# Performance work log

Hardware: AMD Instinct MI355X
Metric: run time of the kernel (lower is better)

## Reference

```python
import jax, jax.numpy as jnp
import numpy as np

B, H, S, D = 4, 16, 1024, 64
MAX_REL = 16  # max_relative_position


def setup_inputs() -> dict:
    key = jax.random.key(0)
    kq, kk, kv, kr = jax.random.split(key, 4)
    Q = jax.random.normal(kq, (B, H, S, D), dtype=jnp.float32)
    K = jax.random.normal(kk, (B, H, S, D), dtype=jnp.float32)
    V = jax.random.normal(kv, (B, H, S, D), dtype=jnp.float32)
    # learned relative-position embedding table [2*P+1, d_k]
    rel_table = jax.random.normal(kr, (2 * MAX_REL + 1, D), dtype=jnp.float32) * 0.02
    # causal mask, broadcastable over batch/heads; 0 => masked
    mask = jnp.tril(jnp.ones((S, S), dtype=jnp.int32))[None, None, :, :]
    return {"Q": Q, "K": K, "V": V, "rel_table": rel_table, "mask": mask}


def reference(Q, K, V, rel_table, mask):
    scale = jnp.sqrt(jnp.asarray(Q.shape[-1], Q.dtype))
    seq_len = Q.shape[2]
    r = jnp.arange(seq_len)
    # clipped relative distances -> embedding indices in [0, 2P]
    idx = jnp.clip(r[None, :] - r[:, None], -MAX_REL, MAX_REL) + MAX_REL  # [S,S]
    rel_emb = rel_table[idx]  # [S, S, D]
    scores = jnp.einsum('bhld,bhrd->bhlr', Q, K) / scale  # [B,H,S,S]
    scores = scores + jnp.einsum('bhld,lrd->bhlr', Q, rel_emb)
    scores = jnp.where(mask == 0, -jnp.inf, scores)
    attn = jax.nn.softmax(scores, axis=-1)
    output = jnp.einsum('bhlr,bhrd->bhld', attn, V)  # [B,H,S,D]
    return (output, attn)
```

## Files before the change

### kernel.cpp

```cpp
#include <hip/hip_runtime.h>

#define S_ 1024
#define D_ 64
#define RT 16
#define SCP 1036

typedef _Float16 f16x4 __attribute__((ext_vector_type(4)));
typedef _Float16 f16x8 __attribute__((ext_vector_type(8)));
typedef __fp16  h16x2 __attribute__((ext_vector_type(2)));
typedef float f32x4 __attribute__((ext_vector_type(4)));

__global__ __launch_bounds__(256)
void prep_kv(const float* __restrict__ K, const float* __restrict__ V,
             _Float16* __restrict__ Kws, _Float16* __restrict__ VT) {
    if (blockIdx.x < 1024) {
        const int idx = blockIdx.x * 256 + threadIdx.x;
        const int g4  = idx & 3;
        const float* kp = K + (size_t)(idx >> 2) * 64 + g4 * 16;
        _Float16* dst = Kws + (size_t)(idx >> 2) * 64 + g4 * 16;
        f16x8 o0, o1;
        #pragma unroll
        for (int u = 0; u < 2; ++u) {
            float4 f0 = *reinterpret_cast<const float4*>(kp + 8 * u);
            float4 f1 = *reinterpret_cast<const float4*>(kp + 8 * u + 4);
            f16x8& o = u ? o1 : o0;
            o[0] = (_Float16)f0.x; o[1] = (_Float16)f0.y;
            o[2] = (_Float16)f0.z; o[3] = (_Float16)f0.w;
            o[4] = (_Float16)f1.x; o[5] = (_Float16)f1.y;
            o[6] = (_Float16)f1.z; o[7] = (_Float16)f1.w;
        }
        *reinterpret_cast<f16x8*>(dst)     = o0;
        *reinterpret_cast<f16x8*>(dst + 8) = o1;
    } else {
        const int idx = (blockIdx.x - 1024) * 256 + threadIdx.x;
        const int bh  = idx >> 12;
        const int kt  = (idx >> 6) & 63;
        const int col = idx & 63;
        const float* vp = V + ((size_t)bh * S_ + kt * 16) * D_ + col;
        _Float16* dst = VT + ((size_t)(bh * 64 + kt) * 64 + col) * 16;
        f16x8 a, b;
        #pragma unroll
        for (int kk = 0; kk < 16; ++kk) {
            float f = vp[(size_t)kk * D_];
            if (kk < 8) a[kk] = (_Float16)f; else b[kk - 8] = (_Float16)f;
        }
        *reinterpret_cast<f16x8*>(dst)     = a;
        *reinterpret_cast<f16x8*>(dst + 8) = b;
    }
}

__global__ __launch_bounds__(256, 4)
void relattn_main(const float* __restrict__ Q, const float* __restrict__ rel,
                  const _Float16* __restrict__ Kws, const _Float16* __restrict__ VT,
                  float* __restrict__ outO, float* outA) {
    __shared__ __align__(16) _Float16 sc[RT * SCP];
    __shared__ float qrel[RT * 17];
    __shared__ float rowsum[4][RT];

    const int tid  = threadIdx.x;
    const int lane = tid & 63;
    const int w    = tid >> 6;
    const int l15  = lane & 15;
    const int g4   = lane >> 4;
    const int bid  = blockIdx.x;
    const int bh   = (bid & 7) + 8 * (bid >> 9);
    const int tile = 63 - ((bid >> 3) & 63);
    const int R0   = tile * RT;
    const int nt16 = tile + 1;
    const int bound = 16 * nt16;

    const float* Qb = Q + (size_t)bh * S_ * D_;
    const _Float16* Kb = Kws + (size_t)bh * 64 * 1024;
    const _Float16* Vt = VT  + (size_t)bh * 64 * 1024;

    {
        const int mend = (bound + 255) & ~255;
        const f16x8 zz = {0, 0, 0, 0, 0, 0, 0, 0};
        const int r = tid >> 4;
        for (int c = bound + (tid & 15) * 8; c < mend; c += 128)
            *reinterpret_cast<f16x8*>(&sc[r * SCP + c]) = zz;
    }

    {
        int idx = tid;
        #pragma unroll
        for (int rep = 0; rep < 2; ++rep) {
            if (idx < RT * 17) {
                const int i = idx / 17;
                const int j = idx - i * 17;
                const float* qp = Qb + (size_t)(R0 + i) * D_;
                const float* rp = rel + j * D_;
                float s = 0.f;
                #pragma unroll
                for (int d = 0; d < D_; d += 4) {
                    float4 a = *reinterpret_cast<const float4*>(qp + d);
                    float4 b = *reinterpret_cast<const float4*>(rp + d);
                    s += a.x * b.x + a.y * b.y + a.z * b.z + a.w * b.w;
                }
                qrel[idx] = s;
            }
            idx = 256 + tid;
        }
    }

    f16x8 aq0, aq1;
    {
        const float* qp = Qb + (size_t)(R0 + l15) * D_ + 8 * g4;
        float4 f0 = *reinterpret_cast<const float4*>(qp);
        float4 f1 = *reinterpret_cast<const float4*>(qp + 4);
        float4 f2 = *reinterpret_cast<const float4*>(qp + 32);
        float4 f3 = *reinterpret_cast<const float4*>(qp + 36);
        aq0 = f16x8{(_Float16)(f0.x*0.125f), (_Float16)(f0.y*0.125f),
                    (_Float16)(f0.z*0.125f), (_Float16)(f0.w*0.125f),
                    (_Float16)(f1.x*0.125f), (_Float16)(f1.y*0.125f),
                    (_Float16)(f1.z*0.125f), (_Float16)(f1.w*0.125f)};
        aq1 = f16x8{(_Float16)(f2.x*0.125f), (_Float16)(f2.y*0.125f),
                    (_Float16)(f2.z*0.125f), (_Float16)(f2.w*0.125f),
                    (_Float16)(f3.x*0.125f), (_Float16)(f3.y*0.125f),
                    (_Float16)(f3.z*0.125f), (_Float16)(f3.w*0.125f)};
    }

    const int myrow   = R0 + l15;
    const int fastmax = (R0 - 31) >> 4;

    auto k_load = [&](int ct, f16x8* kf) {
        const _Float16* kp = Kb + ((size_t)ct * 16 + l15) * 64 + 8 * g4;
        kf[0] = *reinterpret_cast<const f16x8*>(kp);
        kf[1] = *reinterpret_cast<const f16x8*>(kp + 32);
    };
    auto v_load = [&](int ct, f16x4* vf) {
        const _Float16* vp = Vt + ((size_t)ct * 64 + l15) * 16 + 4 * g4;
        #pragma unroll
        for (int n = 0; n < 4; ++n)
            vf[n] = *reinterpret_cast<const f16x4*>(vp + (size_t)n * 256);
    };
    auto load2 = [&](int ct0, f16x8* kf, f16x4* vf) {
        k_load(ct0, kf);
        v_load(ct0, vf);
        if (ct0 + 4 < nt16) { k_load(ct0 + 4, kf + 2); v_load(ct0 + 4, vf + 4); }
    };

    f16x8 kA[4], kB[4];
    f16x4 vA[8], vB[8];
    load2(w, kA, vA);

    __syncthreads();

    const float qr0 = qrel[l15 * 17];
    float psum = 0.f;
    f32x4 oa[4] = {{0,0,0,0},{0,0,0,0},{0,0,0,0},{0,0,0,0}};

    auto comp_tile = [&](int ct, const f16x8* kf, const f16x4* vf) {
        f32x4 acc = {0.f, 0.f, 0.f, 0.f};
        acc = __builtin_amdgcn_mfma_f32_16x16x32_f16(kf[0], aq0, acc, 0, 0, 0);
        acc = __builtin_amdgcn_mfma_f32_16x16x32_f16(kf[1], aq1, acc, 0, 0, 0);
        float e[4];
        if (ct <= fastmax) {
            #pragma unroll
            for (int j = 0; j < 4; ++j) e[j] = __expf(acc[j] + qr0);
        } else {
            #pragma unroll
            for (int j = 0; j < 4; ++j) {
                const int dlt = myrow - (ct * 16 + 4 * g4 + j);
                e[j] = 0.f;
                if (dlt >= 0)
                    e[j] = __expf(acc[j] + ((dlt < 16) ? qrel[l15 * 17 + 16 - dlt]
                                                       : qr0));
            }
        }
        psum += (e[0] + e[1]) + (e[2] + e[3]);
        h16x2 lo = __builtin_amdgcn_cvt_pkrtz(e[0], e[1]);
        h16x2 hi = __builtin_amdgcn_cvt_pkrtz(e[2], e[3]);
        f16x4 pk = {(_Float16)lo[0], (_Float16)lo[1],
                    (_Float16)hi[0], (_Float16)hi[1]};
        *reinterpret_cast<f16x4*>(&sc[l15 * SCP + ct * 16 + 4 * g4]) = pk;
        #pragma unroll
        for (int n = 0; n < 4; ++n)
            oa[n] = __builtin_amdgcn_mfma_f32_16x16x16f16(pk, vf[n], oa[n], 0, 0, 0);
    };
    auto comp2 = [&](int ct0, const f16x8* kf, const f16x4* vf) {
        comp_tile(ct0, kf, vf);
        if (ct0 + 4 < nt16) comp_tile(ct0 + 4, kf + 2, vf + 4);
    };

    for (int c0 = w; c0 < nt16; c0 += 16) {
        if (c0 + 8 < nt16) load2(c0 + 8, kB, vB);
        comp2(c0, kA, vA);
        if (c0 + 8 < nt16) {
            if (c0 + 16 < nt16) load2(c0 + 16, kA, vA);
            comp2(c0 + 8, kB, vB);
        }
    }

    psum += __shfl_xor(psum, 16);
    psum += __shfl_xor(psum, 32);
    if (lane < 16) rowsum[w][lane] = psum;
    __syncthreads();

    float* Ab = outA + ((size_t)bh * S_ + R0) * S_;
    #pragma unroll
    for (int ii = 0; ii < 4; ++ii) {
        const int i = 4 * w + ii;
        const float iv = 1.f / (rowsum[0][i] + rowsum[1][i] +
                                rowsum[2][i] + rowsum[3][i]);
        #pragma unroll
        for (int q = 0; q < 4; ++q) {
            const int c = q * 256 + lane * 4;
            f32x4 o = {0.f, 0.f, 0.f, 0.f};
            if (q * 256 < bound) {
                f16x4 sv = *reinterpret_cast<f16x4*>(&sc[i * SCP + c]);
                o = {(float)sv[0] * iv, (float)sv[1] * iv,
                     (float)sv[2] * iv, (float)sv[3] * iv};
            }
            __builtin_nontemporal_store(
                o, reinterpret_cast<f32x4*>(Ab + (size_t)i * S_ + c));
        }
    }

    __syncthreads();

    float* Opart = reinterpret_cast<float*>(sc);
    #pragma unroll
    for (int n = 0; n < 4; ++n)
        #pragma unroll
        for (int j = 0; j < 4; ++j)
            Opart[((w * 16) + (4 * g4 + j)) * 64 + 16 * n + l15] = oa[n][j];
    __syncthreads();

    float* Ob = outO + (size_t)bh * S_ * D_;
    #pragma unroll
    for (int ii = 0; ii < 4; ++ii) {
        const int row = 4 * w + ii;
        const float s = rowsum[0][row] + rowsum[1][row] +
                        rowsum[2][row] + rowsum[3][row];
        const float o = Opart[(0 * 16 + row) * 64 + lane] +
                        Opart[(1 * 16 + row) * 64 + lane] +
                        Opart[(2 * 16 + row) * 64 + lane] +
                        Opart[(3 * 16 + row) * 64 + lane];
        Ob[(size_t)(R0 + row) * D_ + lane] = o / s;
    }
}

extern "C" void kernel_launch(void* const* d_in, const int* in_sizes, int n_in,
                              void* d_out, int out_size, void* d_ws, size_t ws_size,
                              hipStream_t stream) {
    const float* Q   = (const float*)d_in[0];
    const float* K   = (const float*)d_in[1];
    const float* V   = (const float*)d_in[2];
    const float* rel = (const float*)d_in[3];

    float* out  = (float*)d_out;
    float* outO = out;
    float* outA = out + (size_t)4 * 16 * 1024 * 64;

    _Float16*  Kws  = (_Float16*)((char*)d_ws + (size_t)(1 << 20));
    _Float16*  VTws = (_Float16*)((char*)d_ws + (size_t)(10 << 20));

    prep_kv<<<dim3(2048), dim3(256), 0, stream>>>(K, V, Kws, VTws);
    relattn_main<<<dim3(4096), dim3(256), 0, stream>>>(Q, rel, Kws, VTws,
                                                       outO, outA);
}
```

Measured before the change: 121.7 us.

## Use 8 waves per block with single-tile software-pipelined K/V prefetch

```diff
diff --git a/kernel.cpp b/kernel.cpp
--- a/kernel.cpp
+++ b/kernel.cpp
@@ -49,13 +49,13 @@
     }
 }
 
-__global__ __launch_bounds__(256, 4)
+__global__ __launch_bounds__(512, 8)
 void relattn_main(const float* __restrict__ Q, const float* __restrict__ rel,
                   const _Float16* __restrict__ Kws, const _Float16* __restrict__ VT,
                   float* __restrict__ outO, float* outA) {
     __shared__ __align__(16) _Float16 sc[RT * SCP];
     __shared__ float qrel[RT * 17];
-    __shared__ float rowsum[4][RT];
+    __shared__ float rowsum[8][RT];
 
     const int tid  = threadIdx.x;
     const int lane = tid & 63;
@@ -75,32 +75,27 @@
 
     {
         const int mend = (bound + 255) & ~255;
-        const f16x8 zz = {0, 0, 0, 0, 0, 0, 0, 0};
-        const int r = tid >> 4;
-        for (int c = bound + (tid & 15) * 8; c < mend; c += 128)
+        const int r = tid >> 5;
+        const int c = bound + (tid & 31) * 8;
+        if (c < mend) {
+            const f16x8 zz = {0, 0, 0, 0, 0, 0, 0, 0};
             *reinterpret_cast<f16x8*>(&sc[r * SCP + c]) = zz;
-    }
-
-    {
-        int idx = tid;
-        #pragma unroll
-        for (int rep = 0; rep < 2; ++rep) {
-            if (idx < RT * 17) {
-                const int i = idx / 17;
-                const int j = idx - i * 17;
-                const float* qp = Qb + (size_t)(R0 + i) * D_;
-                const float* rp = rel + j * D_;
-                float s = 0.f;
-                #pragma unroll
-                for (int d = 0; d < D_; d += 4) {
-                    float4 a = *reinterpret_cast<const float4*>(qp + d);
-                    float4 b = *reinterpret_cast<const float4*>(rp + d);
-                    s += a.x * b.x + a.y * b.y + a.z * b.z + a.w * b.w;
-                }
-                qrel[idx] = s;
-            }
-            idx = 256 + tid;
-        }
+        }
+    }
+
+    if (tid < RT * 17) {
+        const int i = tid / 17;
+        const int j = tid - i * 17;
+        const float* qp = Qb + (size_t)(R0 + i) * D_;
+        const float* rp = rel + j * D_;
+        float s = 0.f;
+        #pragma unroll
+        for (int d = 0; d < D_; d += 4) {
+            float4 a = *reinterpret_cast<const float4*>(qp + d);
+            float4 b = *reinterpret_cast<const float4*>(rp + d);
+            s += a.x * b.x + a.y * b.y + a.z * b.z + a.w * b.w;
+        }
+        qrel[tid] = s;
     }
 
     f16x8 aq0, aq1;
@@ -123,37 +118,36 @@
     const int myrow   = R0 + l15;
     const int fastmax = (R0 - 31) >> 4;
 
-    auto k_load = [&](int ct, f16x8* kf) {
-        const _Float16* kp = Kb + ((size_t)ct * 16 + l15) * 64 + 8 * g4;
-        kf[0] = *reinterpret_cast<const f16x8*>(kp);
-        kf[1] = *reinterpret_cast<const f16x8*>(kp + 32);
-    };
-    auto v_load = [&](int ct, f16x4* vf) {
-        const _Float16* vp = Vt + ((size_t)ct * 64 + l15) * 16 + 4 * g4;
-        #pragma unroll
-        for (int n = 0; n < 4; ++n)
-            vf[n] = *reinterpret_cast<const f16x4*>(vp + (size_t)n * 256);
-    };
-    auto load2 = [&](int ct0, f16x8* kf, f16x4* vf) {
-        k_load(ct0, kf);
-        v_load(ct0, vf);
-        if (ct0 + 4 < nt16) { k_load(ct0 + 4, kf + 2); v_load(ct0 + 4, vf + 4); }
-    };
-
-    f16x8 kA[4], kB[4];
-    f16x4 vA[8], vB[8];
-    load2(w, kA, vA);
+    f16x8 kA0, kA1;
+    f16x4 vA0, vA1, vA2, vA3;
+    if (w < nt16) {
+        const _Float16* kp = Kb + ((size_t)w * 16 + l15) * 64 + 8 * g4;
+        kA0 = *reinterpret_cast<const f16x8*>(kp);
+        kA1 = *reinterpret_cast<const f16x8*>(kp + 32);
+        const _Float16* vp = Vt + ((size_t)w * 64 + l15) * 16 + 4 * g4;
+        vA0 = *reinterpret_cast<const f16x4*>(vp);
+        vA1 = *reinterpret_cast<const f16x4*>(vp + 256);
+        vA2 = *reinterpret_cast<const f16x4*>(vp + 512);
+        vA3 = *reinterpret_cast<const f16x4*>(vp + 768);
+    }
 
     __syncthreads();
 
     const float qr0 = qrel[l15 * 17];
     float psum = 0.f;
-    f32x4 oa[4] = {{0,0,0,0},{0,0,0,0},{0,0,0,0},{0,0,0,0}};
-
-    auto comp_tile = [&](int ct, const f16x8* kf, const f16x4* vf) {
+    f32x4 oa0 = {0,0,0,0}, oa1 = {0,0,0,0}, oa2 = {0,0,0,0}, oa3 = {0,0,0,0};
+
+    for (int ct = w; ct < nt16; ct += 8) {
         f32x4 acc = {0.f, 0.f, 0.f, 0.f};
-        acc = __builtin_amdgcn_mfma_f32_16x16x32_f16(kf[0], aq0, acc, 0, 0, 0);
-        acc = __builtin_amdgcn_mfma_f32_16x16x32_f16(kf[1], aq1, acc, 0, 0, 0);
+        acc = __builtin_amdgcn_mfma_f32_16x16x32_f16(kA0, aq0, acc, 0, 0, 0);
+        acc = __builtin_amdgcn_mfma_f32_16x16x32_f16(kA1, aq1, acc, 0, 0, 0);
+        const int  nct  = ct + 8;
+        const bool more = nct < nt16;
+        if (more) {
+            const _Float16* kp = Kb + ((size_t)nct * 16 + l15) * 64 + 8 * g4;
+            kA0 = *reinterpret_cast<const f16x8*>(kp);
+            kA1 = *reinterpret_cast<const f16x8*>(kp + 32);
+        }
         float e[4];
         if (ct <= fastmax) {
             #pragma unroll
@@ -174,21 +168,16 @@
         f16x4 pk = {(_Float16)lo[0], (_Float16)lo[1],
                     (_Float16)hi[0], (_Float16)hi[1]};
         *reinterpret_cast<f16x4*>(&sc[l15 * SCP + ct * 16 + 4 * g4]) = pk;
-        #pragma unroll
-        for (int n = 0; n < 4; ++n)
-            oa[n] = __builtin_amdgcn_mfma_f32_16x16x16f16(pk, vf[n], oa[n], 0, 0, 0);
-    };
-    auto comp2 = [&](int ct0, const f16x8* kf, const f16x4* vf) {
-        comp_tile(ct0, kf, vf);
-        if (ct0 + 4 < nt16) comp_tile(ct0 + 4, kf + 2, vf + 4);
-    };
-
-    for (int c0 = w; c0 < nt16; c0 += 16) {
-        if (c0 + 8 < nt16) load2(c0 + 8, kB, vB);
-        comp2(c0, kA, vA);
-        if (c0 + 8 < nt16) {
-            if (c0 + 16 < nt16) load2(c0 + 16, kA, vA);
-            comp2(c0 + 8, kB, vB);
+        oa0 = __builtin_amdgcn_mfma_f32_16x16x16f16(pk, vA0, oa0, 0, 0, 0);
+        oa1 = __builtin_amdgcn_mfma_f32_16x16x16f16(pk, vA1, oa1, 0, 0, 0);
+        oa2 = __builtin_amdgcn_mfma_f32_16x16x16f16(pk, vA2, oa2, 0, 0, 0);
+        oa3 = __builtin_amdgcn_mfma_f32_16x16x16f16(pk, vA3, oa3, 0, 0, 0);
+        if (more) {
+            const _Float16* vp = Vt + ((size_t)nct * 64 + l15) * 16 + 4 * g4;
+            vA0 = *reinterpret_cast<const f16x4*>(vp);
+            vA1 = *reinterpret_cast<const f16x4*>(vp + 256);
+            vA2 = *reinterpret_cast<const f16x4*>(vp + 512);
+            vA3 = *reinterpret_cast<const f16x4*>(vp + 768);
         }
     }
 
@@ -199,10 +188,12 @@
 
     float* Ab = outA + ((size_t)bh * S_ + R0) * S_;
     #pragma unroll
-    for (int ii = 0; ii < 4; ++ii) {
-        const int i = 4 * w + ii;
-        const float iv = 1.f / (rowsum[0][i] + rowsum[1][i] +
-                                rowsum[2][i] + rowsum[3][i]);
+    for (int ii = 0; ii < 2; ++ii) {
+        const int i = 2 * w + ii;
+        float s = 0.f;
+        #pragma unroll
+        for (int p = 0; p < 8; ++p) s += rowsum[p][i];
+        const float iv = 1.f / s;
         #pragma unroll
         for (int q = 0; q < 4; ++q) {
             const int c = q * 256 + lane * 4;
@@ -220,23 +211,37 @@
     __syncthreads();
 
     float* Opart = reinterpret_cast<float*>(sc);
-    #pragma unroll
-    for (int n = 0; n < 4; ++n)
-        #pragma unroll
-        for (int j = 0; j < 4; ++j)
-            Opart[((w * 16) + (4 * g4 + j)) * 64 + 16 * n + l15] = oa[n][j];
+    {
+        const int r0 = 4 * g4;
+        Opart[((w * 16) + r0 + 0) * 64 + 16 * 0 + l15] = oa0[0];
+        Opart[((w * 16) + r0 + 1) * 64 + 16 * 0 + l15] = oa0[1];
+        Opart[((w * 16) + r0 + 2) * 64 + 16 * 0 + l15] = oa0[2];
+        Opart[((w * 16) + r0 + 3) * 64 + 16 * 0 + l15] = oa0[3];
+        Opart[((w * 16) + r0 + 0) * 64 + 16 * 1 + l15] = oa1[0];
+        Opart[((w * 16) + r0 + 1) * 64 + 16 * 1 + l15] = oa1[1];
+        Opart[((w * 16) + r0 + 2) * 64 + 16 * 1 + l15] = oa1[2];
+        Opart[((w * 16) + r0 + 3) * 64 + 16 * 1 + l15] = oa1[3];
+        Opart[((w * 16) + r0 + 0) * 64 + 16 * 2 + l15] = oa2[0];
+        Opart[((w * 16) + r0 + 1) * 64 + 16 * 2 + l15] = oa2[1];
+        Opart[((w * 16) + r0 + 2) * 64 + 16 * 2 + l15] = oa2[2];
+        Opart[((w * 16) + r0 + 3) * 64 + 16 * 2 + l15] = oa2[3];
+        Opart[((w * 16) + r0 + 0) * 64 + 16 * 3 + l15] = oa3[0];
+        Opart[((w * 16) + r0 + 1) * 64 + 16 * 3 + l15] = oa3[1];
+        Opart[((w * 16) + r0 + 2) * 64 + 16 * 3 + l15] = oa3[2];
+        Opart[((w * 16) + r0 + 3) * 64 + 16 * 3 + l15] = oa3[3];
+    }
     __syncthreads();
 
     float* Ob = outO + (size_t)bh * S_ * D_;
     #pragma unroll
-    for (int ii = 0; ii < 4; ++ii) {
-        const int row = 4 * w + ii;
-        const float s = rowsum[0][row] + rowsum[1][row] +
-                        rowsum[2][row] + rowsum[3][row];
-        const float o = Opart[(0 * 16 + row) * 64 + lane] +
-                        Opart[(1 * 16 + row) * 64 + lane] +
-                        Opart[(2 * 16 + row) * 64 + lane] +
-                        Opart[(3 * 16 + row) * 64 + lane];
+    for (int ii = 0; ii < 2; ++ii) {
+        const int row = 2 * w + ii;
+        float s = 0.f, o = 0.f;
+        #pragma unroll
+        for (int p = 0; p < 8; ++p) {
+            s += rowsum[p][row];
+            o += Opart[(p * 16 + row) * 64 + lane];
+        }
         Ob[(size_t)(R0 + row) * D_ + lane] = o / s;
     }
 }
@@ -257,6 +262,6 @@
     _Float16*  VTws = (_Float16*)((char*)d_ws + (size_t)(10 << 20));
 
     prep_kv<<<dim3(2048), dim3(256), 0, stream>>>(K, V, Kws, VTws);
-    relattn_main<<<dim3(4096), dim3(256), 0, stream>>>(Q, rel, Kws, VTws,
+    relattn_main<<<dim3(4096), dim3(512), 0, stream>>>(Q, rel, Kws, VTws,
                                                        outO, outA);
 }
```

Measured after the change: 136.1 us. +11.8%, slower.
